# Optimization experiments

Measured on AMD Instinct MI355X. Metric: run time of the kernel, lower is better.

## Reference

```python
import jax, jax.numpy as jnp
import numpy as np

B, D = 8192, 64


def _mlp(x, w1, b1, w2, b2):
    # Linear -> exact GELU (torch nn.GELU default) -> Linear
    h = jax.nn.gelu(x @ w1 + b1, approximate=False)
    return h @ w2 + b2


def setup_inputs() -> dict:
    key = jax.random.key(0)
    ks = jax.random.split(key, 16)
    def lin(k, fan_in, fan_out):
        return jax.random.normal(k, (fan_in, fan_out), jnp.float32) / np.sqrt(fan_in).astype(np.float32)
    inp = {"z": jax.random.normal(ks[0], (B, 81, D), jnp.float32)}
    for i, name in enumerate(["row", "col", "box"]):
        inp[f"{name}_w1"] = lin(ks[1 + 4 * i], 9 * D, D)
        inp[f"{name}_b1"] = jnp.zeros((D,), jnp.float32)
        inp[f"{name}_w2"] = lin(ks[2 + 4 * i], D, D)
        inp[f"{name}_b2"] = jnp.zeros((D,), jnp.float32)
    inp["gate_w"] = lin(ks[13], 3 * D, D)
    inp["gate_b"] = jnp.zeros((D,), jnp.float32)
    inp["alpha"] = jnp.float32(0.1)
    return inp


def reference(z, row_w1, row_b1, row_w2, row_b2,
              col_w1, col_b1, col_w2, col_b2,
              box_w1, box_b1, box_w2, box_b2,
              gate_w, gate_b, alpha):
    Bv = z.shape[0]
    z_grid = z.reshape(Bv, 9, 9, D)
    # row context: each of 9 rows flattened -> (B, 9, 9D)
    row_ctx = z_grid.reshape(Bv, 9, 9 * D)
    row_up = _mlp(row_ctx, row_w1, row_b1, row_w2, row_b2)[:, :, None, :]  # (B,9,1,D)
    # col context: transpose rows/cols then flatten -> (B, 9, 9D)
    col_ctx = jnp.transpose(z_grid, (0, 2, 1, 3)).reshape(Bv, 9, 9 * D)
    col_up = _mlp(col_ctx, col_w1, col_b1, col_w2, col_b2)[:, None, :, :]  # (B,1,9,D)
    # box context: (B,3,3,3,3,D) -> (B, br, bc, r, c, D) -> (B, 9, 9D)
    box_ctx = jnp.transpose(z_grid.reshape(Bv, 3, 3, 3, 3, D), (0, 1, 3, 2, 4, 5)).reshape(Bv, 9, 9 * D)
    box_up = _mlp(box_ctx, box_w1, box_b1, box_w2, box_b2).reshape(Bv, 3, 3, D)
    # replicate exact torch expand+reshape semantics (mixes d and inner-col axes)
    box_up = jnp.broadcast_to(box_up[:, :, :, None, :, None], (Bv, 3, 3, 3, D, 3)).reshape(Bv, 9, 9, D)
    row_upb = jnp.broadcast_to(row_up, (Bv, 9, 9, D))
    col_upb = jnp.broadcast_to(col_up, (Bv, 9, 9, D))
    delta_sum = row_upb + col_upb + box_up
    gate_in = jnp.concatenate([row_upb, col_upb, box_up], axis=-1)  # (B,9,9,3D)
    gate = jax.nn.sigmoid(gate_in @ gate_w + gate_b)  # (B,9,9,D)
    z_new = z_grid + alpha * gate * delta_sum
    return z_new.reshape(Bv, 81, D)
```

## Files before the change

kernel.cpp:

```cpp
#include <hip/hip_runtime.h>
#include <hip/hip_bf16.h>

typedef __attribute__((ext_vector_type(8))) short short8;
typedef __attribute__((ext_vector_type(4))) short short4v;
typedef __attribute__((ext_vector_type(4))) float f32x4;

__device__ __forceinline__ unsigned short f2bf(float f) {
    union { __hip_bfloat16 b; unsigned short u; } v;
    v.b = __float2bfloat16(f);
    return v.u;
}
__device__ __forceinline__ float bf2f(unsigned short u) {
    return __uint_as_float(((unsigned)u) << 16);
}
__device__ __forceinline__ float gelu_tanh(float x) {
    float u = 0.79788456080286536f * x * (1.0f + 0.044715f * x * x);
    return x * __builtin_amdgcn_rcpf(1.0f + __builtin_exp2f(-2.8853900817779268f * u));
}
__device__ __forceinline__ float sigmoidf(float x) {
    return __builtin_amdgcn_rcpf(1.0f + __builtin_exp2f(-1.4426950408889634f * x));
}
__device__ __forceinline__ int swz(int row, int col) {
    return (row * 64 + col) ^ ((row & 7) << 3);
}

__global__ __launch_bounds__(256)
void prepack_kernel(const float* __restrict__ w1r, const float* __restrict__ w1c,
                    const float* __restrict__ w1b,
                    const float* __restrict__ w2r, const float* __restrict__ w2c,
                    const float* __restrict__ w2b,
                    const float* __restrict__ gw, unsigned short* __restrict__ ws)
{
    int t = blockIdx.x * 256 + threadIdx.x;
    if (t < 13824) {
        int wi = t / 4608, r = t % 4608;
        const float* src = (wi == 0) ? w1r : (wi == 1) ? w1c : w1b;
        unsigned short* dst = ws + wi * 36864;
        int lane = r & 63;
        int col = ((r >> 6) & 3) * 16 + (lane & 15);
        int k0 = (r >> 8) * 32 + (lane >> 4) * 8;
        #pragma unroll
        for (int j = 0; j < 8; ++j) dst[r * 8 + j] = f2bf(src[(k0 + j) * 64 + col]);
    } else if (t < 15360) {
        int q = t - 13824, wi = q / 512, r = q % 512;
        const float* src = (wi == 0) ? w2r : (wi == 1) ? w2c : w2b;
        unsigned short* dst = ws + 110592 + wi * 4096;
        int lane = r & 63;
        int col = ((r >> 6) & 3) * 16 + (lane & 15);
        int k0 = (r >> 8) * 32 + (lane >> 4) * 8;
        #pragma unroll
        for (int j = 0; j < 8; ++j) dst[r * 8 + j] = f2bf(src[(k0 + j) * 64 + col]);
    } else if (t < 17920) {
        int r = t - 15360;
        unsigned short* dst = ws + 122880;
        int lane = r & 63;
        int col = ((r >> 6) & 3) * 16 + (lane & 15);
        int k0 = (r >> 8) * 32 + (lane >> 4) * 8;
        #pragma unroll
        for (int j = 0; j < 8; ++j) {
            int krow = k0 + j;
            float v;
            if (krow < 128) {
                v = gw[krow * 64 + col];
            } else {
                int c = (krow - 128) >> 6, e = (krow - 128) & 63;
                int lo = 3 * e - 64 * c;
                v = 0.f;
                #pragma unroll
                for (int s = 0; s < 3; ++s) {
                    int dp = lo + s;
                    if (dp >= 0 && dp < 64) v += gw[(128 + dp) * 64 + col];
                }
            }
            dst[r * 8 + j] = f2bf(v);
        }
    }
}

#define UPWS_OFF 147456

__global__ __launch_bounds__(256, 3)
void k1_mlp(const float* __restrict__ z,
            const float* __restrict__ b1r, const float* __restrict__ b2r,
            const float* __restrict__ b1c, const float* __restrict__ b2c,
            const float* __restrict__ b1b, const float* __restrict__ b2b,
            const short* __restrict__ wsp, unsigned short* __restrict__ upws)
{
    __shared__ __align__(16) unsigned short zl[20736];
    __shared__ __align__(16) unsigned short hlds[4096];
    const int t = threadIdx.x;
    const int lane = t & 63;
    const int w = t >> 6;
    const int rl = lane & 15;
    const int kg = lane >> 4;
    const int b0 = blockIdx.x * 4;
    const int hoff = w * 1024;

    {
        const float* src = z + (size_t)b0 * 5184;
        for (int g = t; g < 5184; g += 256) {
            float4 v = *(const float4*)(src + g * 4);
            int row = g >> 4;
            int col = (g & 15) * 4;
            uint2 pk;
            pk.x = ((unsigned)f2bf(v.y) << 16) | f2bf(v.x);
            pk.y = ((unsigned)f2bf(v.w) << 16) | f2bf(v.z);
            *(uint2*)&zl[swz(row, col)] = pk;
        }
    }
    __syncthreads();

    for (int tt = w; tt < 9; tt += 4) {
        const int type = tt / 3, pg = tt % 3;
        const int b = rl & 3, js = rl >> 2;
        const int jraw = 4 * pg + js;
        const int j = (jraw < 9) ? jraw : 8;
        const int cellbase = (type == 0) ? j * 9
                           : (type == 1) ? j
                           :               (j / 3) * 27 + (j % 3) * 3;
        const int rowbase = b * 81 + cellbase;

        const short* w1p = wsp + type * 36864;
        const short* w2p = wsp + 110592 + type * 4096;
        const float* b1p = (type == 0) ? b1r : (type == 1) ? b1c : b1b;
        const float* b2p = (type == 0) ? b2r : (type == 1) ? b2c : b2b;
        float b1v[4], b2v[4];
        #pragma unroll
        for (int nt = 0; nt < 4; ++nt) { b1v[nt] = b1p[nt * 16 + rl]; b2v[nt] = b2p[nt * 16 + rl]; }

        f32x4 acc[4];
        #pragma unroll
        for (int nt = 0; nt < 4; ++nt) acc[nt] = (f32x4)0.f;

        #pragma unroll
        for (int kk = 0; kk < 18; ++kk) {
            const int s = kk >> 1;
            const int sadd = (type == 0) ? s : (type == 1) ? 9 * s : (s / 3) * 9 + (s % 3);
            const int feat = (kk & 1) * 32 + kg * 8;
            short8 a = *(const short8*)&zl[swz(rowbase + sadd, feat)];
            #pragma unroll
            for (int nt = 0; nt < 4; ++nt) {
                short8 bv = *(const short8*)(w1p + ((kk * 4 + nt) * 64 + lane) * 8);
                acc[nt] = __builtin_amdgcn_mfma_f32_16x16x32_bf16(a, bv, acc[nt], 0, 0, 0);
            }
        }

        asm volatile("s_waitcnt lgkmcnt(0)" ::: "memory");
        #pragma unroll
        for (int nt = 0; nt < 4; ++nt)
            #pragma unroll
            for (int reg = 0; reg < 4; ++reg)
                hlds[hoff + swz(kg * 4 + reg, nt * 16 + rl)] =
                    f2bf(gelu_tanh(acc[nt][reg] + b1v[nt]));
        asm volatile("s_waitcnt lgkmcnt(0)" ::: "memory");

        f32x4 a2c[4];
        #pragma unroll
        for (int nt = 0; nt < 4; ++nt) a2c[nt] = (f32x4)0.f;
        #pragma unroll
        for (int kk2 = 0; kk2 < 2; ++kk2) {
            short8 a2 = *(const short8*)&hlds[hoff + swz(rl, kk2 * 32 + kg * 8)];
            #pragma unroll
            for (int nt = 0; nt < 4; ++nt) {
                short8 bw = *(const short8*)(w2p + ((kk2 * 4 + nt) * 64 + lane) * 8);
                a2c[nt] = __builtin_amdgcn_mfma_f32_16x16x32_bf16(a2, bw, a2c[nt], 0, 0, 0);
            }
        }
        asm volatile("s_waitcnt lgkmcnt(0)" ::: "memory");
        #pragma unroll
        for (int nt = 0; nt < 4; ++nt)
            #pragma unroll
            for (int reg = 0; reg < 4; ++reg)
                hlds[hoff + swz(kg * 4 + reg, nt * 16 + rl)] = f2bf(a2c[nt][reg] + b2v[nt]);
        asm volatile("s_waitcnt lgkmcnt(0)" ::: "memory");

        #pragma unroll
        for (int p2 = 0; p2 < 2; ++p2) {
            const int hrow = p2 * 8 + (lane >> 3), f0 = (lane & 7) * 8;
            const int sjs = hrow >> 2, sb = hrow & 3;
            const int sj = 4 * pg + sjs;
            if (sj < 9) {
                short8 v = *(const short8*)&hlds[hoff + swz(hrow, f0)];
                *(short8*)(upws + ((size_t)(b0 + sb) * 27 + type * 9 + sj) * 64 + f0) = v;
            }
        }
    }
}

__global__ __launch_bounds__(576, 4)
void k2_gate(const float* __restrict__ z, const unsigned short* __restrict__ upws,
             const short* __restrict__ wsp, const float* __restrict__ gb,
             const float* __restrict__ alphap, float* __restrict__ out)
{
    __shared__ __align__(16) unsigned short ups[27648];
    __shared__ __align__(16) unsigned short tscr[9][1024];
    const int t = threadIdx.x;
    const int lane = t & 63;
    const int w = t >> 6;
    const int rl = lane & 15;
    const int kg = lane >> 4;
    const int b0 = blockIdx.x * 16;

    #pragma unroll
    for (int c6 = 0; c6 < 6; ++c6) {
        int chunk = t + c6 * 576;
        int row = chunk >> 3, f0 = (chunk & 7) * 8;
        short8 v = *(const short8*)(upws + (size_t)b0 * 1728 + chunk * 8);
        *(short8*)&ups[swz(row, f0)] = v;
    }
    __syncthreads();

    const short* gwp = wsp + 122880;
    const float alpha = alphap[0];
    float gbl[4][4];
    #pragma unroll
    for (int mt = 0; mt < 4; ++mt)
        #pragma unroll
        for (int reg = 0; reg < 4; ++reg) gbl[mt][reg] = gb[mt * 16 + kg * 4 + reg];

    const int c = w % 3, wg = w / 3;

    #pragma unroll
    for (int tl = 0; tl < 9; ++tl) {
        int e = (wg * 9 + tl) * 16 + rl;
        int b = e / 27, rem = e % 27, R = rem / 3, q = rem % 3, C = c + 3 * q;
        int rowR = b * 27 + R, rowC = b * 27 + 9 + C, rowB = b * 27 + 18 + R;

        f32x4 acc[4];
        #pragma unroll
        for (int mt = 0; mt < 4; ++mt) acc[mt] = (f32x4)0.f;

        #pragma unroll
        for (int s6 = 0; s6 < 6; ++s6) {
            int seg = s6 >> 1;
            int kkp = (s6 < 4) ? s6 : 4 + 2 * c + (s6 - 4);
            int row = (seg == 0) ? rowR : (seg == 1) ? rowC : rowB;
            int f = (s6 & 1) * 32 + kg * 8;
            short8 bfrag = *(const short8*)&ups[swz(row, f)];
            #pragma unroll
            for (int mt = 0; mt < 4; ++mt) {
                short8 afrag = *(const short8*)(gwp + ((kkp * 4 + mt) * 64 + lane) * 8);
                acc[mt] = __builtin_amdgcn_mfma_f32_16x16x32_bf16(afrag, bfrag, acc[mt], 0, 0, 0);
            }
        }

        #pragma unroll
        for (int mt = 0; mt < 4; ++mt) {
            short4v du4 = *(const short4v*)&ups[swz(rowR, mt * 16 + kg * 4)];
            short4v dc4 = *(const short4v*)&ups[swz(rowC, mt * 16 + kg * 4)];
            #pragma unroll
            for (int reg = 0; reg < 4; ++reg) {
                int fidx = mt * 16 + kg * 4 + reg;
                float g = sigmoidf(acc[mt][reg] + gbl[mt][reg]);
                float duv = bf2f((unsigned short)du4[reg]);
                float dcv = bf2f((unsigned short)dc4[reg]);
                float dbv = bf2f(ups[swz(rowB, (64 * c + fidx) / 3)]);
                tscr[w][swz(rl, fidx)] = f2bf(alpha * g * (duv + dcv + dbv));
            }
        }
        asm volatile("s_waitcnt lgkmcnt(0)" ::: "memory");
        #pragma unroll
        for (int p = 0; p < 2; ++p) {
            int cl = p * 8 + (lane >> 3), f0 = (lane & 7) * 8;
            int e2 = (wg * 9 + tl) * 16 + cl;
            int b2 = e2 / 27, rem2 = e2 % 27, R2 = rem2 / 3, C2 = c + 3 * (rem2 % 3);
            short8 tv = *(const short8*)&tscr[w][swz(cl, f0)];
            const float* zp = z + (size_t)(b0 + b2) * 5184 + (size_t)(R2 * 9 + C2) * 64 + f0;
            float4 z0 = *(const float4*)zp;
            float4 z1 = *(const float4*)(zp + 4);
            float4 o0, o1;
            o0.x = z0.x + bf2f((unsigned short)tv[0]);
            o0.y = z0.y + bf2f((unsigned short)tv[1]);
            o0.z = z0.z + bf2f((unsigned short)tv[2]);
            o0.w = z0.w + bf2f((unsigned short)tv[3]);
            o1.x = z1.x + bf2f((unsigned short)tv[4]);
            o1.y = z1.y + bf2f((unsigned short)tv[5]);
            o1.z = z1.z + bf2f((unsigned short)tv[6]);
            o1.w = z1.w + bf2f((unsigned short)tv[7]);
            float* op = out + (size_t)(b0 + b2) * 5184 + (size_t)(R2 * 9 + C2) * 64 + f0;
            *(float4*)op = o0;
            *(float4*)(op + 4) = o1;
        }
        asm volatile("s_waitcnt lgkmcnt(0)" ::: "memory");
    }
}

extern "C" void kernel_launch(void* const* d_in, const int* in_sizes, int n_in,
                              void* d_out, int out_size, void* d_ws, size_t ws_size,
                              hipStream_t stream) {
    const float* z   = (const float*)d_in[0];
    const float* w1r = (const float*)d_in[1];
    const float* b1r = (const float*)d_in[2];
    const float* w2r = (const float*)d_in[3];
    const float* b2r = (const float*)d_in[4];
    const float* w1c = (const float*)d_in[5];
    const float* b1c = (const float*)d_in[6];
    const float* w2c = (const float*)d_in[7];
    const float* b2c = (const float*)d_in[8];
    const float* w1b = (const float*)d_in[9];
    const float* b1b = (const float*)d_in[10];
    const float* w2b = (const float*)d_in[11];
    const float* b2b = (const float*)d_in[12];
    const float* gw  = (const float*)d_in[13];
    const float* gb  = (const float*)d_in[14];
    const float* al  = (const float*)d_in[15];
    float* outp = (float*)d_out;
    unsigned short* ws = (unsigned short*)d_ws;

    prepack_kernel<<<70, 256, 0, stream>>>(w1r, w1c, w1b, w2r, w2c, w2b, gw, ws);

    const int Btot = in_sizes[0] / 5184;
    unsigned short* upws = ws + UPWS_OFF;
    k1_mlp<<<Btot / 4, 256, 0, stream>>>(z, b1r, b2r, b1c, b2c, b1b, b2b,
                                         (const short*)ws, upws);
    k2_gate<<<Btot / 16, 576, 0, stream>>>(z, upws, (const short*)ws, gb, al, outp);
}
```

Before: 195.2 us.

## Split MLP kernel by context type and keep weights in registers

k1_mlp now launches three blocks per group of 4 batches, one per row/col/box type. Each wave owns a 16-column N slice and preloads its W1 and W2 fragments and biases into registers once, instead of re-reading weights from global memory inside the tile loop. The cost is that each block still stages the full z tile for its 4 batches, so z is loaded and converted to bf16 three times across the grid. Block-wide __syncthreads now replace the per-wave LDS scratch synchronisation.

```diff
diff --git a/kernel.cpp b/kernel.cpp
--- a/kernel.cpp
+++ b/kernel.cpp
@@ -87,14 +87,31 @@
             const short* __restrict__ wsp, unsigned short* __restrict__ upws)
 {
     __shared__ __align__(16) unsigned short zl[20736];
-    __shared__ __align__(16) unsigned short hlds[4096];
+    __shared__ __align__(16) unsigned short hl[1024];
+    __shared__ __align__(16) unsigned short ub[1024];
     const int t = threadIdx.x;
     const int lane = t & 63;
     const int w = t >> 6;
     const int rl = lane & 15;
     const int kg = lane >> 4;
-    const int b0 = blockIdx.x * 4;
-    const int hoff = w * 1024;
+    const int type = blockIdx.x % 3;
+    const int b0 = (blockIdx.x / 3) * 4;
+
+    const short* w1p = wsp + type * 36864;
+    const short* w2p = wsp + 110592 + type * 4096;
+    const float* b1p = (type == 0) ? b1r : (type == 1) ? b1c : b1b;
+    const float* b2p = (type == 0) ? b2r : (type == 1) ? b2c : b2b;
+
+    short8 w1f[18];
+    #pragma unroll
+    for (int kk = 0; kk < 18; ++kk)
+        w1f[kk] = *(const short8*)(w1p + ((kk * 4 + w) * 64 + lane) * 8);
+    short8 w2f[2];
+    #pragma unroll
+    for (int kk2 = 0; kk2 < 2; ++kk2)
+        w2f[kk2] = *(const short8*)(w2p + ((kk2 * 4 + w) * 64 + lane) * 8);
+    const float b1s = b1p[w * 16 + rl];
+    const float b2s = b2p[w * 16 + rl];
 
     {
         const float* src = z + (size_t)b0 * 5184;
@@ -110,77 +127,50 @@
     }
     __syncthreads();
 
-    for (int tt = w; tt < 9; tt += 4) {
-        const int type = tt / 3, pg = tt % 3;
-        const int b = rl & 3, js = rl >> 2;
-        const int jraw = 4 * pg + js;
+    const int b = rl & 3, js = rl >> 2;
+
+    for (int p = 0; p < 3; ++p) {
+        const int jraw = 4 * p + js;
         const int j = (jraw < 9) ? jraw : 8;
         const int cellbase = (type == 0) ? j * 9
                            : (type == 1) ? j
                            :               (j / 3) * 27 + (j % 3) * 3;
         const int rowbase = b * 81 + cellbase;
 
-        const short* w1p = wsp + type * 36864;
-        const short* w2p = wsp + 110592 + type * 4096;
-        const float* b1p = (type == 0) ? b1r : (type == 1) ? b1c : b1b;
-        const float* b2p = (type == 0) ? b2r : (type == 1) ? b2c : b2b;
-        float b1v[4], b2v[4];
-        #pragma unroll
-        for (int nt = 0; nt < 4; ++nt) { b1v[nt] = b1p[nt * 16 + rl]; b2v[nt] = b2p[nt * 16 + rl]; }
-
-        f32x4 acc[4];
-        #pragma unroll
-        for (int nt = 0; nt < 4; ++nt) acc[nt] = (f32x4)0.f;
-
-        #pragma unroll
-        for (int kk = 0; kk < 18; ++kk) {
-            const int s = kk >> 1;
-            const int sadd = (type == 0) ? s : (type == 1) ? 9 * s : (s / 3) * 9 + (s % 3);
-            const int feat = (kk & 1) * 32 + kg * 8;
-            short8 a = *(const short8*)&zl[swz(rowbase + sadd, feat)];
-            #pragma unroll
-            for (int nt = 0; nt < 4; ++nt) {
-                short8 bv = *(const short8*)(w1p + ((kk * 4 + nt) * 64 + lane) * 8);
-                acc[nt] = __builtin_amdgcn_mfma_f32_16x16x32_bf16(a, bv, acc[nt], 0, 0, 0);
-            }
-        }
-
-        asm volatile("s_waitcnt lgkmcnt(0)" ::: "memory");
-        #pragma unroll
-        for (int nt = 0; nt < 4; ++nt)
-            #pragma unroll
-            for (int reg = 0; reg < 4; ++reg)
-                hlds[hoff + swz(kg * 4 + reg, nt * 16 + rl)] =
-                    f2bf(gelu_tanh(acc[nt][reg] + b1v[nt]));
-        asm volatile("s_waitcnt lgkmcnt(0)" ::: "memory");
-
-        f32x4 a2c[4];
-        #pragma unroll
-        for (int nt = 0; nt < 4; ++nt) a2c[nt] = (f32x4)0.f;
+        f32x4 acc0 = (f32x4)0.f, acc1 = (f32x4)0.f;
+        #pragma unroll
+        for (int kk = 0; kk < 18; kk += 2) {
+            const int s0 = kk >> 1;
+            const int sadd = (type == 0) ? s0 : (type == 1) ? 9 * s0 : (s0 / 3) * 9 + (s0 % 3);
+            short8 a0 = *(const short8*)&zl[swz(rowbase + sadd, kg * 8)];
+            short8 a1 = *(const short8*)&zl[swz(rowbase + sadd, 32 + kg * 8)];
+            acc0 = __builtin_amdgcn_mfma_f32_16x16x32_bf16(a0, w1f[kk],     acc0, 0, 0, 0);
+            acc1 = __builtin_amdgcn_mfma_f32_16x16x32_bf16(a1, w1f[kk + 1], acc1, 0, 0, 0);
+        }
+
+        #pragma unroll
+        for (int reg = 0; reg < 4; ++reg)
+            hl[swz(kg * 4 + reg, w * 16 + rl)] =
+                f2bf(gelu_tanh(acc0[reg] + acc1[reg] + b1s));
+        __syncthreads();
+
+        f32x4 a2c = (f32x4)0.f;
         #pragma unroll
         for (int kk2 = 0; kk2 < 2; ++kk2) {
-            short8 a2 = *(const short8*)&hlds[hoff + swz(rl, kk2 * 32 + kg * 8)];
-            #pragma unroll
-            for (int nt = 0; nt < 4; ++nt) {
-                short8 bw = *(const short8*)(w2p + ((kk2 * 4 + nt) * 64 + lane) * 8);
-                a2c[nt] = __builtin_amdgcn_mfma_f32_16x16x32_bf16(a2, bw, a2c[nt], 0, 0, 0);
-            }
-        }
-        asm volatile("s_waitcnt lgkmcnt(0)" ::: "memory");
-        #pragma unroll
-        for (int nt = 0; nt < 4; ++nt)
-            #pragma unroll
-            for (int reg = 0; reg < 4; ++reg)
-                hlds[hoff + swz(kg * 4 + reg, nt * 16 + rl)] = f2bf(a2c[nt][reg] + b2v[nt]);
-        asm volatile("s_waitcnt lgkmcnt(0)" ::: "memory");
-
-        #pragma unroll
-        for (int p2 = 0; p2 < 2; ++p2) {
-            const int hrow = p2 * 8 + (lane >> 3), f0 = (lane & 7) * 8;
-            const int sjs = hrow >> 2, sb = hrow & 3;
-            const int sj = 4 * pg + sjs;
+            short8 a2 = *(const short8*)&hl[swz(rl, kk2 * 32 + kg * 8)];
+            a2c = __builtin_amdgcn_mfma_f32_16x16x32_bf16(a2, w2f[kk2], a2c, 0, 0, 0);
+        }
+        #pragma unroll
+        for (int reg = 0; reg < 4; ++reg)
+            ub[swz(kg * 4 + reg, w * 16 + rl)] = f2bf(a2c[reg] + b2s);
+        __syncthreads();
+
+        if (w < 2) {
+            const int hrow = w * 8 + (lane >> 3), f0 = (lane & 7) * 8;
+            const int sb = hrow & 3, sjs = hrow >> 2;
+            const int sj = 4 * p + sjs;
             if (sj < 9) {
-                short8 v = *(const short8*)&hlds[hoff + swz(hrow, f0)];
+                short8 v = *(const short8*)&ub[swz(hrow, f0)];
                 *(short8*)(upws + ((size_t)(b0 + sb) * 27 + type * 9 + sj) * 64 + f0) = v;
             }
         }
@@ -311,7 +301,7 @@
 
     const int Btot = in_sizes[0] / 5184;
     unsigned short* upws = ws + UPWS_OFF;
-    k1_mlp<<<Btot / 4, 256, 0, stream>>>(z, b1r, b2r, b1c, b2c, b1b, b2b,
-                                         (const short*)ws, upws);
+    k1_mlp<<<(Btot / 4) * 3, 256, 0, stream>>>(z, b1r, b2r, b1c, b2c, b1b, b2b,
+                                               (const short*)ws, upws);
     k2_gate<<<Btot / 16, 576, 0, stream>>>(z, upws, (const short*)ws, gb, al, outp);
 }
```

Result: slower. 210.8 us (+8.0%).
